# Optimization experiments

Hardware: AMD Instinct MI355X
Metric: run time of the kernel (lower is better)

The kernel has to match this reference:

```python
import jax, jax.numpy as jnp
import numpy as np

K = 2        # kernel_size
DIL = 1      # dilation
H = 768      # h_size = nhid + nout
NOUT = 256
NLAYER = 10  # weight-tied iterations of f_theta


def conv1d(x, w, b, dilation=1):
    # x: (B, Cin, L), w: (Cout, Cin, K) -> (B, Cout, L-(K-1)*dilation)
    y = jax.lax.conv_general_dilated(
        x, w, window_strides=(1,), padding='VALID',
        rhs_dilation=(dilation,), dimension_numbers=('NCH', 'OIH', 'NCH'))
    return y + b[None, :, None]


def setup_inputs() -> dict:
    key = jax.random.key(0)
    ks = jax.random.split(key, 5)
    B, NINP, L = 4, 512, 1024
    bound = 0.01  # init_weights() uses N(0, 0.01)
    return {
        'X': jax.random.normal(ks[0], (B, NINP, L), dtype=jnp.float32),
        'z0': jnp.zeros((B, 2 * H, 1), dtype=jnp.float32),
        'inject_w': bound * jax.random.normal(ks[1], (4 * H, NINP, K), dtype=jnp.float32),
        'inject_b': bound * jax.random.normal(ks[2], (4 * H,), dtype=jnp.float32),
        'conv_w': bound * jax.random.normal(ks[3], (4 * H, H, K), dtype=jnp.float32),
        'conv_b': bound * jax.random.normal(ks[4], (4 * H,), dtype=jnp.float32),
    }


def reference(X, z0, inject_w, inject_b, conv_w, conv_b):
    B, _, L = X.shape
    pad_in = K - 1            # inject conv causal padding
    pad_h = (K - 1) * DIL     # hidden conv causal padding

    # us = inject_conv(pad(X)) : (B, 4H, L), computed once
    Xp = jnp.pad(X, ((0, 0), (0, 0), (pad_in, 0)))
    us = conv1d(Xp, inject_w, inject_b, dilation=1)

    z0h, z0c = z0[:, :H], z0[:, H:]  # (B, H, 1) each
    hid_pad = jnp.broadcast_to(z0h, (B, H, pad_h))  # repeat history into padding

    def step(z1s, _):
        z1h, z1c = z1s[:, :H], z1s[:, H:]
        # shifted cell state: cat([z0c, z1c])[:, :, :-1]
        z0c_s = jnp.concatenate([z0c, z1c[:, :, :-1]], axis=2)
        # weight-tied causal dilated conv on hidden part, history in padding
        xh = jnp.concatenate([hid_pad, z1h], axis=2)
        out = us + conv1d(xh, conv_w, conv_b, dilation=DIL)  # (B, 4H, L)
        it, ot, gt, ft = jnp.split(out, 4, axis=1)
        ct = jax.nn.sigmoid(ft) * z0c_s + jax.nn.sigmoid(it) * jnp.tanh(gt)
        ht = jax.nn.sigmoid(ot) * jnp.tanh(ct)
        return jnp.concatenate([ht, ct], axis=1), None

    z1s0 = jnp.zeros((B, 2 * H, L), dtype=X.dtype)
    z1s, _ = jax.lax.scan(step, z1s0, None, length=NLAYER)

    out = jnp.transpose(z1s[:, H - NOUT:H], (0, 2, 1))  # (B, L, nout)
    z0_out = z1s[:, :, -1:]                              # history repackaging
    return out, z0_out
```

## Files before the change

### kernel.cpp

```cpp
#include <hip/hip_runtime.h>
#include <hip/hip_bf16.h>
#include <stdint.h>


#define B_    4
#define L_    1024
#define LP1   1025
#define H_    768
#define NG_   3072
#define NINP_ 512
#define NOUT_ 256

typedef __bf16 bf16x8 __attribute__((ext_vector_type(8)));
typedef float f32x4 __attribute__((ext_vector_type(4)));
typedef _Float16 f16x4 __attribute__((ext_vector_type(4)));
using bf16_t = __hip_bfloat16;

__device__ __forceinline__ float sigf(float x){ return 1.f/(1.f + __expf(-x)); }
__device__ __forceinline__ float tanhf_(float x){
  float e = __expf(-2.f*fabsf(x));
  float r = (1.f - e)/(1.f + e);
  return x >= 0.f ? r : -r;
}

__device__ __forceinline__ void gl_lds16(const void* g, void* l){
  __builtin_amdgcn_global_load_lds(
    (const __attribute__((address_space(1))) uint32_t*)g,
    (__attribute__((address_space(3))) uint32_t*)l, 16, 0, 0);
}

__device__ __forceinline__ size_t htile_idx(int b, int t, int j){
  return ((size_t)((b*64 + (t>>4))*24) + (j>>5))*512
         + (size_t)((t&15)*8 + ((j>>3)&3)*128 + (j&7));
}

__global__ void init_k(const float* __restrict__ z0, bf16_t* __restrict__ XB,
                       bf16_t* __restrict__ HB0, bf16_t* __restrict__ HB1,
                       _Float16* __restrict__ C0, _Float16* __restrict__ C1){
  int tid = blockIdx.x*256 + threadIdx.x;
  if (tid < B_*NINP_){
    int b = tid >> 9, r = tid & 511;
    int kb = r>>5, lk = (r>>3)&3, e = r&7;
    XB[((size_t)(b*64*16) + kb)*512 + lk*128 + e] = __float2bfloat16(0.f);
  }
  if (tid < B_*H_){
    int b = tid / H_, j = tid % H_;
    bf16_t hz = __float2bfloat16(z0[b*2*H_ + j]);
    _Float16 cz = (_Float16)z0[b*2*H_ + H_ + j];
    size_t a = ((size_t)(b*64*24) + (j>>5))*512 + ((j>>3)&3)*128 + (j&7);
    HB0[a] = hz; HB1[a] = hz;
    size_t idx = (size_t)b*LP1*H_ + j;
    C0[idx] = cz; C1[idx] = cz;
  }
}

__global__ void prep_w(const float* __restrict__ iw, const float* __restrict__ ib,
                       const float* __restrict__ cw, const float* __restrict__ cb,
                       bf16_t* __restrict__ WitT, bf16_t* __restrict__ WctT,
                       float* __restrict__ bias4){
  int op = blockIdx.x;
  int gate = (op >> 4) & 3;
  int j = ((op >> 6) << 4) | (op & 15);
  int o = gate*H_ + j;
  int nt = op >> 4, lrow = op & 15;
  const float2* s2 = (const float2*)(iw + (size_t)o*NINP_*2);
  for (int i = threadIdx.x; i < NINP_; i += 256){
    float2 v = s2[i];
    int k0 = i, k1 = NINP_ + i;
    WitT[((size_t)(nt*32 + (k0>>5)))*512 + lrow*8 + ((k0>>3)&3)*128 + (k0&7)] = __float2bfloat16(v.x);
    WitT[((size_t)(nt*32 + (k1>>5)))*512 + lrow*8 + ((k1>>3)&3)*128 + (k1&7)] = __float2bfloat16(v.y);
  }
  const float2* c2 = (const float2*)(cw + (size_t)o*H_*2);
  for (int i = threadIdx.x; i < H_; i += 256){
    float2 v = c2[i];
    int k0 = i, k1 = H_ + i;
    WctT[((size_t)(nt*48 + (k0>>5)))*512 + lrow*8 + ((k0>>3)&3)*128 + (k0&7)] = __float2bfloat16(v.x);
    WctT[((size_t)(nt*48 + (k1>>5)))*512 + lrow*8 + ((k1>>3)&3)*128 + (k1&7)] = __float2bfloat16(v.y);
  }
  if (threadIdx.x == 0) bias4[j*4 + gate] = ib[o] + cb[o];
}

__global__ void tile_x(const float* __restrict__ X, bf16_t* __restrict__ XA,
                       bf16_t* __restrict__ XB){
  int b = blockIdx.z, i = blockIdx.y;
  int t = blockIdx.x*256 + threadIdx.x;
  bf16_t bv = __float2bfloat16(X[((size_t)b*NINP_ + i)*L_ + t]);
  int kb = i>>5, lk = (i>>3)&3, e = i&7;
  XA[((size_t)((b*64 + (t>>4))*16) + kb)*512 + (t&15)*8 + lk*128 + e] = bv;
  if (t < L_-1){
    int t1 = t + 1;
    XB[((size_t)((b*64 + (t1>>4))*16) + kb)*512 + (t1&15)*8 + lk*128 + e] = bv;
  }
}

template<int KTOT, int MODE>
__launch_bounds__(256, 3)
__global__ void gemmF(const bf16_t* __restrict__ A1, const bf16_t* __restrict__ A0,
                      const bf16_t* __restrict__ Bt, const float* __restrict__ bias4,
                      f16x4* __restrict__ us4, const _Float16* __restrict__ Cprev,
                      _Float16* __restrict__ Cnew, bf16_t* __restrict__ HAn,
                      bf16_t* __restrict__ HBn, float* __restrict__ outF, int bn_base){
  __shared__ __align__(1024) char smem[49152];

  const int tid = threadIdx.x;
  const int l  = tid & 63;
  const int w  = tid >> 6;
  const int wm = w >> 1, wn = w & 1;
  const int lr = l & 15;
  const int lk = l >> 4;

  const int nwg = gridDim.x * gridDim.y;
  int flat = blockIdx.y * gridDim.x + blockIdx.x;
  flat = (flat & 7) * (nwg >> 3) + (flat >> 3);
  const int bm0 = (flat & 31) * 128;
  const int bn0 = bn_base + (flat >> 5) * 128;

  f32x4 acc[4][4];
#pragma unroll
  for (int i = 0; i < 4; ++i)
#pragma unroll
    for (int jj = 0; jj < 4; ++jj)
      acc[i][jj] = (f32x4){0.f,0.f,0.f,0.f};

  constexpr int KB0 = (KTOT == 1024) ? 16 : 24;
  constexpr int KBB = KTOT / 32;
  const int bI = bm0 >> 10;
  const int g0 = (bm0 >> 4) & 63;

  const char* a0p[2]; const char* a1p[2]; const char* bp[2];
#pragma unroll
  for (int n = 0; n < 2; ++n){
    const int g = g0 + w*2 + n;
    a0p[n] = (const char*)A0 + (((size_t)(bI*64 + g)*KB0) << 10) + l*16;
    a1p[n] = (const char*)A1 + (((size_t)(bI*64 + g)*KB0) << 10) + l*16;
    const int nt = (bn0 >> 4) + w*2 + n;
    bp[n]  = (const char*)Bt + (((size_t)nt*KBB) << 10) + l*16;
  }
  const int a0off = (w*2    )*1024;
  const int a1off = (w*2 + 1)*1024;

#define STAGE_AT(S, T) { \
    char* base_ = smem + (S)*16384; \
    const int T_ = (T); \
    const size_t koA = (size_t)(T_ < KB0 ? T_ : T_ - KB0) << 10; \
    const char* as0 = (T_ < KB0) ? a0p[0] : a1p[0]; \
    const char* as1 = (T_ < KB0) ? a0p[1] : a1p[1]; \
    gl_lds16(as0 + koA, base_ + a0off); \
    gl_lds16(as1 + koA, base_ + a1off); \
    gl_lds16(bp[0] + ((size_t)T_ << 10), base_ + 8192 + a0off); \
    gl_lds16(bp[1] + ((size_t)T_ << 10), base_ + 8192 + a1off); }

#define COMPUTE_AT(S) { \
    const char* sp_ = smem + (S)*16384 + l*16; \
    bf16x8 af[4], bv[4]; \
    _Pragma("unroll") for (int f = 0; f < 4; ++f) \
      af[f] = *(const bf16x8*)(sp_ + (wm*4 + f)*1024); \
    _Pragma("unroll") for (int f = 0; f < 4; ++f) \
      bv[f] = *(const bf16x8*)(sp_ + 8192 + (wn*4 + f)*1024); \
    __builtin_amdgcn_s_setprio(1); \
    _Pragma("unroll") for (int fm = 0; fm < 4; ++fm) \
      _Pragma("unroll") for (int fn = 0; fn < 4; ++fn) \
        acc[fm][fn] = __builtin_amdgcn_mfma_f32_16x16x32_bf16(af[fm], bv[fn], acc[fm][fn], 0, 0, 0); \
    __builtin_amdgcn_s_setprio(0); }

  constexpr int NT = KTOT / 32;

  STAGE_AT(0, 0)
  STAGE_AT(1, 1)
  int slot = 0;
  for (int t = 0; t < NT; ++t){
    if (t < NT - 1) { asm volatile("s_waitcnt vmcnt(4)" ::: "memory"); }
    else            { asm volatile("s_waitcnt vmcnt(0)" ::: "memory"); }
    __builtin_amdgcn_s_barrier();
    if (t + 2 < NT){
      const int s2 = (slot >= 1) ? slot - 1 : 2;
      STAGE_AT(s2, t + 2)
    }
    COMPUTE_AT(slot)
    slot = (slot < 2) ? slot + 1 : 0;
  }

#undef STAGE_AT
#undef COMPUTE_AT

  const int jblk = (bn0 >> 6) + wn;
  const int j = jblk*16 + lr;
  const int rq = lk << 2;

  if (MODE == 0){
    const float4 bz = ((const float4*)bias4)[j];
#pragma unroll
    for (int fm = 0; fm < 4; ++fm){
      const int mbase = bm0 + wm*64 + fm*16 + rq;
#pragma unroll
      for (int r = 0; r < 4; ++r){
        const int m = mbase + r;
        const int b = m >> 10, t = m & 1023;
        const float ig = acc[fm][0][r] + bz.x;
        const float og = acc[fm][1][r] + bz.y;
        const float gg = acc[fm][2][r] + bz.z;
        const float fg = acc[fm][3][r] + bz.w;
        us4[(size_t)m*H_ + j] = (f16x4){ (_Float16)ig, (_Float16)og,
                                         (_Float16)gg, (_Float16)fg };
        const float cp = (t == 0) ? (float)Cprev[(size_t)b*LP1*H_ + j] : 0.f;
        const float c  = sigf(fg)*cp + sigf(ig)*tanhf_(gg);
        const float h  = sigf(og)*tanhf_(c);
        Cnew[(size_t)(b*LP1 + t + 1)*H_ + j] = (_Float16)c;
        bf16_t hb = __float2bfloat16(h);
        HAn[htile_idx(b, t, j)] = hb;
        if (t < L_-1) HBn[htile_idx(b, t+1, j)] = hb;
      }
    }
  } else {
    f16x4 uv[4][4]; _Float16 cp16[4][4];
#pragma unroll
    for (int fm = 0; fm < 4; ++fm){
      const int mbase = bm0 + wm*64 + fm*16 + rq;
#pragma unroll
      for (int r = 0; r < 4; ++r){
        const int m = mbase + r;
        const int b = m >> 10, t = m & 1023;
        uv[fm][r]   = us4[(size_t)m*H_ + j];
        cp16[fm][r] = Cprev[(size_t)(b*LP1 + t)*H_ + j];
      }
    }
#pragma unroll
    for (int fm = 0; fm < 4; ++fm){
      const int mbase = bm0 + wm*64 + fm*16 + rq;
#pragma unroll
      for (int r = 0; r < 4; ++r){
        const int m = mbase + r;
        const int b = m >> 10, t = m & 1023;
        const float ig = acc[fm][0][r] + (float)uv[fm][r][0];
        const float og = acc[fm][1][r] + (float)uv[fm][r][1];
        const float gg = acc[fm][2][r] + (float)uv[fm][r][2];
        const float fg = acc[fm][3][r] + (float)uv[fm][r][3];
        const float c  = sigf(fg)*(float)cp16[fm][r] + sigf(ig)*tanhf_(gg);
        const float h  = sigf(og)*tanhf_(c);
        if (MODE == 1){
          Cnew[(size_t)(b*LP1 + t + 1)*H_ + j] = (_Float16)c;
          bf16_t hb = __float2bfloat16(h);
          HAn[htile_idx(b, t, j)] = hb;
          if (t < L_-1) HBn[htile_idx(b, t+1, j)] = hb;
        } else {
          outF[(size_t)(b*1024 + t)*NOUT_ + (j - (H_ - NOUT_))] = h;
        }
      }
    }
  }
}

__global__ void tail_k(const bf16_t* __restrict__ HA9, const bf16_t* __restrict__ HB9,
                       const _Float16* __restrict__ C9, const f16x4* __restrict__ us4,
                       const bf16_t* __restrict__ WctT, float* __restrict__ out){
  __shared__ float red[4][64];
  const int b = blockIdx.y;
  const int ob = blockIdx.x;
  const int opl = threadIdx.x & 63;
  const int q   = threadIdx.x >> 6;
  const int nt = ob*4 + (opl >> 4);
  const int lr = opl & 15;

  const bf16_t* hsrcb = (q < 2) ? HB9 : HA9;
  const int j0q = (q < 2) ? q*384 : (q-2)*384;
  const size_t gbase = (size_t)(b*64 + 63) * 24;
  const bf16_t* wbase = WctT + ((size_t)(nt*48 + ((q*384)>>5)))*512 + lr*8;

  float s = 0.f;
#pragma unroll 4
  for (int i = 0; i < 48; ++i){
    const int koff = i*8;
    const int j = j0q + koff;
    bf16x8 wv = *reinterpret_cast<const bf16x8*>(wbase + (koff>>5)*512 + ((koff>>3)&3)*128);
    bf16x8 hv = *reinterpret_cast<const bf16x8*>(hsrcb + (gbase + (j>>5))*512 + 120 + ((j>>3)&3)*128);
#pragma unroll
    for (int u = 0; u < 8; ++u) s += (float)hv[u]*(float)wv[u];
  }
  red[q][opl] = s;
  __syncthreads();
  if (threadIdx.x < 64){
    const int gate = (opl >> 4) & 3;
    const int j = ob*16 + lr;
    float sv = red[0][opl] + red[1][opl] + red[2][opl] + red[3][opl];
    sv += (float)us4[(size_t)(b*1024 + 1023)*H_ + j][gate];
    const float si = __shfl(sv, lr);
    const float so = __shfl(sv, lr + 16);
    const float sg = __shfl(sv, lr + 32);
    const float sf = __shfl(sv, lr + 48);
    if (gate == 0){
      const float cp = (float)C9[(size_t)(b*LP1 + 1023)*H_ + j];
      const float c = sigf(sf)*cp + sigf(si)*tanhf_(sg);
      const float h = sigf(so)*tanhf_(c);
      out[B_*L_*NOUT_ + b*2*H_ + j]      = h;
      out[B_*L_*NOUT_ + b*2*H_ + H_ + j] = c;
    }
  }
}

extern "C" void kernel_launch(void* const* d_in, const int* in_sizes, int n_in,
                              void* d_out, int out_size, void* d_ws, size_t ws_size,
                              hipStream_t stream){
  const float* X   = (const float*)d_in[0];
  const float* z0  = (const float*)d_in[1];
  const float* iw  = (const float*)d_in[2];
  const float* ib  = (const float*)d_in[3];
  const float* cw  = (const float*)d_in[4];
  const float* cbv = (const float*)d_in[5];
  float* out = (float*)d_out;

  char* ws = (char*)d_ws;
  f16x4*    us4  = (f16x4*)   (ws + 0);
  bf16_t*   XA   = (bf16_t*)  (ws + 25165824);
  bf16_t*   XB   = (bf16_t*)  (ws + 29360128);
  bf16_t*   WitT = (bf16_t*)  (ws + 33554432);
  bf16_t*   WctT = (bf16_t*)  (ws + 39845888);
  float*    bias4= (float*)   (ws + 49283072);
  bf16_t*   HA0  = (bf16_t*)  (ws + 49295360);
  bf16_t*   HB0  = (bf16_t*)  (ws + 55586816);
  bf16_t*   HA1  = (bf16_t*)  (ws + 61878272);
  bf16_t*   HB1  = (bf16_t*)  (ws + 68169728);
  _Float16* C0   = (_Float16*)(ws + 74461184);
  _Float16* C1   = (_Float16*)(ws + 80758784);

  init_k<<<12, 256, 0, stream>>>(z0, XB, HB0, HB1, C0, C1);
  prep_w<<<NG_, 256, 0, stream>>>(iw, ib, cw, cbv, WitT, WctT, bias4);
  tile_x<<<dim3(4, NINP_, B_), 256, 0, stream>>>(X, XA, XB);

  gemmF<1024, 0><<<dim3(32, 24), 256, 0, stream>>>(
      XA, XB, WitT, bias4, us4, C0, C0, HA0, HB0, nullptr, 0);

  bf16_t* HAp = HA0; bf16_t* HBp = HB0; _Float16* Cp = C0;
  bf16_t* HAn = HA1; bf16_t* HBn = HB1; _Float16* Cn = C1;
  for (int it = 1; it <= 8; ++it){
    gemmF<1536, 1><<<dim3(32, 24), 256, 0, stream>>>(
        HAp, HBp, WctT, nullptr, us4, Cp, Cn, HAn, HBn, nullptr, 0);
    bf16_t* ta = HAp; HAp = HAn; HAn = ta;
    bf16_t* tb = HBp; HBp = HBn; HBn = tb;
    _Float16* tc = Cp; Cp = Cn; Cn = tc;
  }

  tail_k<<<dim3(48, B_), 256, 0, stream>>>(HAp, HBp, Cp, us4, WctT, out);

  gemmF<1536, 2><<<dim3(32, 8), 256, 0, stream>>>(
      HAp, HBp, WctT, nullptr, us4, Cp, nullptr, nullptr, nullptr, out, 2048);
}
```

Measured before the change: 570.8 us.

## Switch GEMM to 256x256 tiles with 8 waves and ping-pong LDS schedule

Replaces the 128x128, 4-wave GEMM with a 256x256 tile computed by 512 threads (8 waves). It uses 128KB of dynamic LDS, double-buffered over 64-wide K steps, and an explicitly interleaved schedule of loads, barriers and MFMA bursts. The larger tile is meant to raise arithmetic intensity and cut redundant global loads. In exchange the grid shrinks to 192 blocks, or 64 for the final projection, which is fewer than the CU count and may underfill the GPU. Register pressure also doubles with 128 accumulator floats per thread.

```diff
diff --git a/kernel.cpp b/kernel.cpp
--- a/kernel.cpp
+++ b/kernel.cpp
@@ -94,112 +94,144 @@
 }
 
 template<int KTOT, int MODE>
-__launch_bounds__(256, 3)
-__global__ void gemmF(const bf16_t* __restrict__ A1, const bf16_t* __restrict__ A0,
+__launch_bounds__(512, 2)
+__global__ void gemm8(const bf16_t* __restrict__ A1, const bf16_t* __restrict__ A0,
                       const bf16_t* __restrict__ Bt, const float* __restrict__ bias4,
                       f16x4* __restrict__ us4, const _Float16* __restrict__ Cprev,
                       _Float16* __restrict__ Cnew, bf16_t* __restrict__ HAn,
                       bf16_t* __restrict__ HBn, float* __restrict__ outF, int bn_base){
-  __shared__ __align__(1024) char smem[49152];
+  extern __shared__ __align__(1024) char smem[];
+  char* ldsA = smem;
+  char* ldsB = smem + 65536;
 
   const int tid = threadIdx.x;
   const int l  = tid & 63;
   const int w  = tid >> 6;
-  const int wm = w >> 1, wn = w & 1;
-  const int lr = l & 15;
-  const int lk = l >> 4;
+  const int wm = w >> 2, wn = w & 3;
+  const int lr = l & 15, lk = l >> 4;
 
   const int nwg = gridDim.x * gridDim.y;
   int flat = blockIdx.y * gridDim.x + blockIdx.x;
   flat = (flat & 7) * (nwg >> 3) + (flat >> 3);
-  const int bm0 = (flat & 31) * 128;
-  const int bn0 = bn_base + (flat >> 5) * 128;
-
-  f32x4 acc[4][4];
-#pragma unroll
-  for (int i = 0; i < 4; ++i)
+  const int bm0 = (flat & 15) * 256;
+  const int bn0 = bn_base + (flat >> 4) * 256;
+
+  constexpr int NT64 = KTOT / 64;
+  constexpr int NI   = NT64 / 2;
+  constexpr int KB0  = (KTOT == 1024) ? 16 : 24;
+  constexpr int KBB  = KTOT / 32;
+
+  f32x4 acc[8][4];
+#pragma unroll
+  for (int i = 0; i < 8; ++i)
 #pragma unroll
     for (int jj = 0; jj < 4; ++jj)
       acc[i][jj] = (f32x4){0.f,0.f,0.f,0.f};
 
-  constexpr int KB0 = (KTOT == 1024) ? 16 : 24;
-  constexpr int KBB = KTOT / 32;
   const int bI = bm0 >> 10;
   const int g0 = (bm0 >> 4) & 63;
-
-  const char* a0p[2]; const char* a1p[2]; const char* bp[2];
+  const char* sA0[2]; const char* sA1[2]; const char* sB[2];
 #pragma unroll
   for (int n = 0; n < 2; ++n){
-    const int g = g0 + w*2 + n;
-    a0p[n] = (const char*)A0 + (((size_t)(bI*64 + g)*KB0) << 10) + l*16;
-    a1p[n] = (const char*)A1 + (((size_t)(bI*64 + g)*KB0) << 10) + l*16;
-    const int nt = (bn0 >> 4) + w*2 + n;
-    bp[n]  = (const char*)Bt + (((size_t)nt*KBB) << 10) + l*16;
-  }
-  const int a0off = (w*2    )*1024;
-  const int a1off = (w*2 + 1)*1024;
-
-#define STAGE_AT(S, T) { \
-    char* base_ = smem + (S)*16384; \
-    const int T_ = (T); \
-    const size_t koA = (size_t)(T_ < KB0 ? T_ : T_ - KB0) << 10; \
-    const char* as0 = (T_ < KB0) ? a0p[0] : a1p[0]; \
-    const char* as1 = (T_ < KB0) ? a0p[1] : a1p[1]; \
-    gl_lds16(as0 + koA, base_ + a0off); \
-    gl_lds16(as1 + koA, base_ + a1off); \
-    gl_lds16(bp[0] + ((size_t)T_ << 10), base_ + 8192 + a0off); \
-    gl_lds16(bp[1] + ((size_t)T_ << 10), base_ + 8192 + a1off); }
-
-#define COMPUTE_AT(S) { \
-    const char* sp_ = smem + (S)*16384 + l*16; \
-    bf16x8 af[4], bv[4]; \
-    _Pragma("unroll") for (int f = 0; f < 4; ++f) \
-      af[f] = *(const bf16x8*)(sp_ + (wm*4 + f)*1024); \
-    _Pragma("unroll") for (int f = 0; f < 4; ++f) \
-      bv[f] = *(const bf16x8*)(sp_ + 8192 + (wn*4 + f)*1024); \
+    const int g = g0 + n*8 + w;
+    sA0[n] = (const char*)A0 + (((size_t)(bI*64 + g)*KB0) << 10) + l*16;
+    sA1[n] = (const char*)A1 + (((size_t)(bI*64 + g)*KB0) << 10) + l*16;
+    const int nt = (bn0 >> 4) + n*8 + w;
+    sB[n]  = (const char*)Bt + (((size_t)nt*KBB) << 10) + l*16;
+  }
+
+#define SA(T, KS, DB) if ((T) < NT64) { \
+    const int kb_ = (T)*2 + (KS); \
+    char* d_ = ldsA + (DB)*32768 + (KS)*16384 + w*1024; \
+    if (kb_ < KB0) { \
+      gl_lds16(sA0[0] + ((size_t)kb_ << 10), d_); \
+      gl_lds16(sA0[1] + ((size_t)kb_ << 10), d_ + 8192); \
+    } else { \
+      gl_lds16(sA1[0] + ((size_t)(kb_ - KB0) << 10), d_); \
+      gl_lds16(sA1[1] + ((size_t)(kb_ - KB0) << 10), d_ + 8192); \
+    } }
+#define SB(T, KS, DB) if ((T) < NT64) { \
+    const int kb_ = (T)*2 + (KS); \
+    char* d_ = ldsB + (DB)*32768 + (KS)*16384 + w*1024; \
+    gl_lds16(sB[0] + ((size_t)kb_ << 10), d_); \
+    gl_lds16(sB[1] + ((size_t)kb_ << 10), d_ + 8192); }
+
+  bf16x8 af[4], bv[4];
+#define RD_B(DB, KS) { \
+    const char* bb_ = ldsB + (DB)*32768 + (KS)*16384 + (wn*4)*1024 + l*16; \
+    bv[0] = *(const bf16x8*)(bb_); \
+    bv[1] = *(const bf16x8*)(bb_ + 1024); \
+    bv[2] = *(const bf16x8*)(bb_ + 2048); \
+    bv[3] = *(const bf16x8*)(bb_ + 3072); }
+#define RD_A(DB, MH, KS) { \
+    const char* ab_ = ldsA + (DB)*32768 + (KS)*16384 + (wm*8 + (MH)*4)*1024 + l*16; \
+    af[0] = *(const bf16x8*)(ab_); \
+    af[1] = *(const bf16x8*)(ab_ + 1024); \
+    af[2] = *(const bf16x8*)(ab_ + 2048); \
+    af[3] = *(const bf16x8*)(ab_ + 3072); }
+
+#define VM8 asm volatile("s_waitcnt vmcnt(8)" ::: "memory");
+#define VM4 asm volatile("s_waitcnt vmcnt(4)" ::: "memory");
+#define VM0 asm volatile("s_waitcnt vmcnt(0)" ::: "memory");
+#define VMN
+
+#define MM(MH, W) \
+    __builtin_amdgcn_s_barrier(); \
+    __builtin_amdgcn_sched_barrier(0); \
     __builtin_amdgcn_s_setprio(1); \
     _Pragma("unroll") for (int fm = 0; fm < 4; ++fm) \
       _Pragma("unroll") for (int fn = 0; fn < 4; ++fn) \
-        acc[fm][fn] = __builtin_amdgcn_mfma_f32_16x16x32_bf16(af[fm], bv[fn], acc[fm][fn], 0, 0, 0); \
-    __builtin_amdgcn_s_setprio(0); }
-
-  constexpr int NT = KTOT / 32;
-
-  STAGE_AT(0, 0)
-  STAGE_AT(1, 1)
-  int slot = 0;
-  for (int t = 0; t < NT; ++t){
-    if (t < NT - 1) { asm volatile("s_waitcnt vmcnt(4)" ::: "memory"); }
-    else            { asm volatile("s_waitcnt vmcnt(0)" ::: "memory"); }
-    __builtin_amdgcn_s_barrier();
-    if (t + 2 < NT){
-      const int s2 = (slot >= 1) ? slot - 1 : 2;
-      STAGE_AT(s2, t + 2)
-    }
-    COMPUTE_AT(slot)
-    slot = (slot < 2) ? slot + 1 : 0;
-  }
-
-#undef STAGE_AT
-#undef COMPUTE_AT
+        acc[(MH)*4 + fm][fn] = __builtin_amdgcn_mfma_f32_16x16x32_bf16(af[fm], bv[fn], acc[(MH)*4 + fm][fn], 0, 0, 0); \
+    __builtin_amdgcn_s_setprio(0); \
+    W \
+    __builtin_amdgcn_s_barrier(); \
+    __builtin_amdgcn_sched_barrier(0);
+
+#define ITER(I, W4, W6, W8) \
+    RD_A(0,0,0) RD_B(0,0) SA(2*(I)+1, 1, 1) MM(0, VMN)    \
+    RD_A(0,1,0)           SB(2*(I)+1, 1, 1) MM(1, VM8)    \
+    RD_A(0,0,1) RD_B(0,1) SA(2*(I)+2, 0, 0) MM(0, VMN)    \
+    RD_A(0,1,1)           SB(2*(I)+2, 0, 0) MM(1, W4)     \
+    RD_A(1,0,0) RD_B(1,0) SA(2*(I)+2, 1, 0) MM(0, VMN)    \
+    RD_A(1,1,0)           SB(2*(I)+2, 1, 0) MM(1, W6)     \
+    RD_A(1,0,1) RD_B(1,1) SA(2*(I)+3, 0, 1) MM(0, VMN)    \
+    RD_A(1,1,1)           SB(2*(I)+3, 0, 1) MM(1, W8)
+
+  SA(0,0,0) SB(0,0,0) SA(0,1,0) SB(0,1,0) SA(1,0,1) SB(1,0,1)
+  VM8
+  __builtin_amdgcn_s_barrier();
+  __builtin_amdgcn_sched_barrier(0);
+
+  for (int i = 0; i < NI-1; ++i){ ITER(i, VM8, VM8, VM8) }
+  { ITER(NI-1, VM4, VM0, VMN) }
+
+#undef SA
+#undef SB
+#undef RD_A
+#undef RD_B
+#undef VM8
+#undef VM4
+#undef VM0
+#undef VMN
+#undef MM
+#undef ITER
 
   const int jblk = (bn0 >> 6) + wn;
   const int j = jblk*16 + lr;
-  const int rq = lk << 2;
 
   if (MODE == 0){
     const float4 bz = ((const float4*)bias4)[j];
 #pragma unroll
-    for (int fm = 0; fm < 4; ++fm){
-      const int mbase = bm0 + wm*64 + fm*16 + rq;
+    for (int mf = 0; mf < 8; ++mf){
+      const int mbase = bm0 + wm*128 + mf*16 + lk*4;
 #pragma unroll
       for (int r = 0; r < 4; ++r){
         const int m = mbase + r;
         const int b = m >> 10, t = m & 1023;
-        const float ig = acc[fm][0][r] + bz.x;
-        const float og = acc[fm][1][r] + bz.y;
-        const float gg = acc[fm][2][r] + bz.z;
-        const float fg = acc[fm][3][r] + bz.w;
+        const float ig = acc[mf][0][r] + bz.x;
+        const float og = acc[mf][1][r] + bz.y;
+        const float gg = acc[mf][2][r] + bz.z;
+        const float fg = acc[mf][3][r] + bz.w;
         us4[(size_t)m*H_ + j] = (f16x4){ (_Float16)ig, (_Float16)og,
                                          (_Float16)gg, (_Float16)fg };
         const float cp = (t == 0) ? (float)Cprev[(size_t)b*LP1*H_ + j] : 0.f;
@@ -212,30 +244,26 @@
       }
     }
   } else {
-    f16x4 uv[4][4]; _Float16 cp16[4][4];
-#pragma unroll
-    for (int fm = 0; fm < 4; ++fm){
-      const int mbase = bm0 + wm*64 + fm*16 + rq;
+#pragma unroll
+    for (int mf = 0; mf < 8; ++mf){
+      const int mbase = bm0 + wm*128 + mf*16 + lk*4;
+      f16x4 uv[4]; _Float16 cp16[4];
 #pragma unroll
       for (int r = 0; r < 4; ++r){
         const int m = mbase + r;
         const int b = m >> 10, t = m & 1023;
-        uv[fm][r]   = us4[(size_t)m*H_ + j];
-        cp16[fm][r] = Cprev[(size_t)(b*LP1 + t)*H_ + j];
+        uv[r]   = us4[(size_t)m*H_ + j];
+        cp16[r] = Cprev[(size_t)(b*LP1 + t)*H_ + j];
       }
-    }
-#pragma unroll
-    for (int fm = 0; fm < 4; ++fm){
-      const int mbase = bm0 + wm*64 + fm*16 + rq;
 #pragma unroll
       for (int r = 0; r < 4; ++r){
         const int m = mbase + r;
         const int b = m >> 10, t = m & 1023;
-        const float ig = acc[fm][0][r] + (float)uv[fm][r][0];
-        const float og = acc[fm][1][r] + (float)uv[fm][r][1];
-        const float gg = acc[fm][2][r] + (float)uv[fm][r][2];
-        const float fg = acc[fm][3][r] + (float)uv[fm][r][3];
-        const float c  = sigf(fg)*(float)cp16[fm][r] + sigf(ig)*tanhf_(gg);
+        const float ig = acc[mf][0][r] + (float)uv[r][0];
+        const float og = acc[mf][1][r] + (float)uv[r][1];
+        const float gg = acc[mf][2][r] + (float)uv[r][2];
+        const float fg = acc[mf][3][r] + (float)uv[r][3];
+        const float c  = sigf(fg)*(float)cp16[r] + sigf(ig)*tanhf_(gg);
         const float h  = sigf(og)*tanhf_(c);
         if (MODE == 1){
           Cnew[(size_t)(b*LP1 + t + 1)*H_ + j] = (_Float16)c;
@@ -322,17 +350,24 @@
   _Float16* C0   = (_Float16*)(ws + 74461184);
   _Float16* C1   = (_Float16*)(ws + 80758784);
 
+  hipFuncSetAttribute((const void*)gemm8<1024,0>,
+                      hipFuncAttributeMaxDynamicSharedMemorySize, 131072);
+  hipFuncSetAttribute((const void*)gemm8<1536,1>,
+                      hipFuncAttributeMaxDynamicSharedMemorySize, 131072);
+  hipFuncSetAttribute((const void*)gemm8<1536,2>,
+                      hipFuncAttributeMaxDynamicSharedMemorySize, 131072);
+
   init_k<<<12, 256, 0, stream>>>(z0, XB, HB0, HB1, C0, C1);
   prep_w<<<NG_, 256, 0, stream>>>(iw, ib, cw, cbv, WitT, WctT, bias4);
   tile_x<<<dim3(4, NINP_, B_), 256, 0, stream>>>(X, XA, XB);
 
-  gemmF<1024, 0><<<dim3(32, 24), 256, 0, stream>>>(
+  gemm8<1024, 0><<<dim3(16, 12), 512, 131072, stream>>>(
       XA, XB, WitT, bias4, us4, C0, C0, HA0, HB0, nullptr, 0);
 
   bf16_t* HAp = HA0; bf16_t* HBp = HB0; _Float16* Cp = C0;
   bf16_t* HAn = HA1; bf16_t* HBn = HB1; _Float16* Cn = C1;
   for (int it = 1; it <= 8; ++it){
-    gemmF<1536, 1><<<dim3(32, 24), 256, 0, stream>>>(
+    gemm8<1536, 1><<<dim3(16, 12), 512, 131072, stream>>>(
         HAp, HBp, WctT, nullptr, us4, Cp, Cn, HAn, HBn, nullptr, 0);
     bf16_t* ta = HAp; HAp = HAn; HAn = ta;
     bf16_t* tb = HBp; HBp = HBn; HBn = tb;
@@ -341,6 +376,6 @@
 
   tail_k<<<dim3(48, B_), 256, 0, stream>>>(HAp, HBp, Cp, us4, WctT, out);
 
-  gemmF<1536, 2><<<dim3(32, 8), 256, 0, stream>>>(
+  gemm8<1536, 2><<<dim3(16, 4), 512, 131072, stream>>>(
       HAp, HBp, WctT, nullptr, us4, Cp, nullptr, nullptr, nullptr, out, 2048);
 }
```

Result: slower. 634.0 us (+11.1%).
